# Kernel optimization log

Measured on AMD Instinct MI355X. Metric: run time of the kernel, lower is better.

The kernel has to match this reference:

```python
import jax, jax.numpy as jnp
import numpy as np

N = 100000
E = 3200000
H = 64

def _lin(k, fan_in, fan_out):
    k1, k2 = jax.random.split(k)
    lim = 1.0 / np.sqrt(fan_in)
    W = jax.random.uniform(k1, (fan_in, fan_out), minval=-lim, maxval=lim, dtype=jnp.float32)
    b = jax.random.uniform(k2, (fan_out,), minval=-lim, maxval=lim, dtype=jnp.float32)
    return W, b

def setup_inputs() -> dict:
    key = jax.random.key(0)
    ks = jax.random.split(key, 12)
    x = jax.random.normal(ks[0], (N, 6), dtype=jnp.float32)
    adj = jax.random.randint(ks[1], (2, E), 0, N, dtype=jnp.int64)
    W1, b1 = _lin(ks[2], 6, H)
    W2, b2 = _lin(ks[3], H, H)
    Wf1, bf1 = _lin(ks[4], H, H)
    Wf2, bf2 = _lin(ks[5], H, H)
    Ws1, bs1 = _lin(ks[6], H, 32)
    Ws2, bs2 = _lin(ks[7], 32, 1)
    Wt1, bt1 = _lin(ks[8], H, 32)
    Wt2, bt2 = _lin(ks[9], 32, 4)
    return dict(x=x, adj=adj, W1=W1, b1=b1, W2=W2, b2=b2, Wf1=Wf1, bf1=bf1,
                Wf2=Wf2, bf2=bf2, Ws1=Ws1, bs1=bs1, Ws2=Ws2, bs2=bs2,
                Wt1=Wt1, bt1=bt1, Wt2=Wt2, bt2=bt2)

def reference(x, adj, W1, b1, W2, b2, Wf1, bf1, Wf2, bf2,
              Ws1, bs1, Ws2, bs2, Wt1, bt1, Wt2, bt2):
    # cell encoder: Linear(6,H) -> ReLU -> Linear(H,H)
    h = jax.nn.relu(x @ W1 + b1) @ W2 + b2  # [N, H]
    # scatter-mean neighbor aggregation: neighbor_sum[i] = mean(h[adj[1][adj[0]==i]])
    src = adj[0]
    dst = adj[1]
    gathered = h[dst]  # [E, H]
    seg_sum = jax.ops.segment_sum(gathered, src, num_segments=N)  # [N, H]
    counts = jax.ops.segment_sum(jnp.ones((E,), dtype=h.dtype), src, num_segments=N)  # [N]
    neighbor_mean = seg_sum / jnp.maximum(counts, 1.0)[:, None]  # zero where no neighbors
    h = h + neighbor_mean
    h = jax.nn.relu(h @ Wf1 + bf1)
    h = jax.nn.relu(h @ Wf2 + bf2)
    error_scores = (jax.nn.relu(h @ Ws1 + bs1) @ Ws2 + bs2)[:, 0]  # [N]
    error_types = jax.nn.relu(h @ Wt1 + bt1) @ Wt2 + bt2  # [N, 4]
    return (error_scores, error_types)
```

## Files before the change

kernel.cpp:

```cpp
#include <hip/hip_runtime.h>
#include <hip/hip_fp16.h>

#define NN 100000
#define NE 3200000
#define H  64

#define BSHIFT 7
#define BNODES 128
#define NB ((NN + BNODES - 1) / BNODES)

#define PTHREADS 1024
#define PCHUNK   8192
#define PEPT     (PCHUNK / PTHREADS)
#define NPBLK    ((NE + PCHUNK - 1) / PCHUNK)

#define ECAP 5120

__global__ __launch_bounds__(256) void prepack_kernel(
    const float* __restrict__ W2,
    const float* __restrict__ Wf1, const float* __restrict__ Wf2,
    const float* __restrict__ Ws1, const float* __restrict__ bs1,
    const float* __restrict__ Ws2, const float* __restrict__ bs2,
    const float* __restrict__ Wt1, const float* __restrict__ bt1,
    const float* __restrict__ Wt2, const float* __restrict__ bt2,
    int* __restrict__ bfill,
    float* __restrict__ wf1t, float* __restrict__ wf2t,
    float* __restrict__ wht,  float* __restrict__ w2t,
    float* __restrict__ bhead, float* __restrict__ wfin, float* __restrict__ bfin)
{
    const int tid = threadIdx.x;
    if (blockIdx.x < 64) {
        const int e   = blockIdx.x * 256 + tid;
        const int a   = e >> 12;
        const int idx = e & 4095;
        const int k4  = idx >> 8;
        const int ff  = (idx >> 2) & 63;
        const int j   = idx & 3;
        if (a == 0)      wf1t[idx] = Wf1[k4 * 256 + j * 64 + ff];
        else if (a == 1) wf2t[idx] = Wf2[k4 * 256 + j * 64 + ff];
        else if (a == 2) wht[idx]  = (ff < 32) ? Ws1[k4 * 128 + j * 32 + ff]
                                               : Wt1[k4 * 128 + j * 32 + (ff - 32)];
        else             w2t[idx]  = W2[k4 * 256 + j * 64 + ff];
    } else {
        for (int i = tid; i < NB; i += 256) bfill[i] = 0;
        if (tid < 64) bhead[tid] = (tid < 32) ? bs1[tid] : bt1[tid - 32];
        if (tid < 160) {
            const int c = tid >> 5, jj = tid & 31;
            wfin[tid] = (c == 0) ? Ws2[jj] : Wt2[jj * 4 + (c - 1)];
        }
        if (tid < 5) bfin[tid] = (tid == 0) ? bs2[0] : bt2[tid - 1];
    }
}

__global__ __launch_bounds__(256) void encoder_kernel(
    const float* __restrict__ x,
    const float* __restrict__ W1, const float* __restrict__ b1,
    const float* __restrict__ w2t, const float* __restrict__ b2,
    __half* __restrict__ h16)
{
    __shared__ float sh[16][H];
    const int tid = threadIdx.x;
    const int w   = tid >> 6;
    const int f   = tid & 63;
    const int nw  = blockIdx.x * 16 + w * 4;

    const float xv = (f < 24) ? x[nw * 6 + f] : 0.0f;

    const float bb1 = b1[f];
    float w1r[6];
    #pragma unroll
    for (int k = 0; k < 6; ++k) w1r[k] = W1[k * H + f];

    #pragma unroll
    for (int j = 0; j < 4; ++j) {
        float acc = bb1;
        #pragma unroll
        for (int k = 0; k < 6; ++k)
            acc = fmaf(__shfl(xv, j * 6 + k), w1r[k], acc);
        sh[w * 4 + j][f] = fmaxf(acc, 0.0f);
    }
    const float bb2 = b2[f];
    float o0 = bb2, o1 = bb2, o2 = bb2, o3 = bb2;
    #pragma unroll
    for (int k4 = 0; k4 < 16; ++k4) {
        const float4 wv = *reinterpret_cast<const float4*>(&w2t[(k4 * 64 + f) * 4]);
        const float4 a0 = *reinterpret_cast<const float4*>(&sh[w * 4 + 0][k4 * 4]);
        const float4 a1 = *reinterpret_cast<const float4*>(&sh[w * 4 + 1][k4 * 4]);
        const float4 a2 = *reinterpret_cast<const float4*>(&sh[w * 4 + 2][k4 * 4]);
        const float4 a3 = *reinterpret_cast<const float4*>(&sh[w * 4 + 3][k4 * 4]);
        o0 = fmaf(a0.x, wv.x, o0); o0 = fmaf(a0.y, wv.y, o0); o0 = fmaf(a0.z, wv.z, o0); o0 = fmaf(a0.w, wv.w, o0);
        o1 = fmaf(a1.x, wv.x, o1); o1 = fmaf(a1.y, wv.y, o1); o1 = fmaf(a1.z, wv.z, o1); o1 = fmaf(a1.w, wv.w, o1);
        o2 = fmaf(a2.x, wv.x, o2); o2 = fmaf(a2.y, wv.y, o2); o2 = fmaf(a2.z, wv.z, o2); o2 = fmaf(a2.w, wv.w, o2);
        o3 = fmaf(a3.x, wv.x, o3); o3 = fmaf(a3.y, wv.y, o3); o3 = fmaf(a3.z, wv.z, o3); o3 = fmaf(a3.w, wv.w, o3);
    }
    h16[((size_t)(nw + 0) << 6) + f] = __float2half(o0);
    h16[((size_t)(nw + 1) << 6) + f] = __float2half(o1);
    h16[((size_t)(nw + 2) << 6) + f] = __float2half(o2);
    h16[((size_t)(nw + 3) << 6) + f] = __float2half(o3);
}

__global__ __launch_bounds__(PTHREADS) void partition_kernel(
    const int* __restrict__ src, const int* __restrict__ dst,
    int* __restrict__ bfill, unsigned* __restrict__ staging)
{
    __shared__ unsigned stage[PCHUNK];
    __shared__ int gpos[PCHUNK];
    __shared__ int lh[NB];
    __shared__ int lcur[NB];
    __shared__ int gbase[NB];
    __shared__ int wtot[16];
    const int t = threadIdx.x;
    const int lane = t & 63;
    const int wid  = t >> 6;
    const int cbase = blockIdx.x * PCHUNK;
    const int cnt = min(PCHUNK, NE - cbase);

    for (int i = t; i < NB; i += PTHREADS) lh[i] = 0;
    __syncthreads();

    unsigned ent[PEPT];
    int bkt[PEPT];
    const int tbase = t * PEPT;
    if (tbase + PEPT <= cnt) {
        const int4 s0 = *reinterpret_cast<const int4*>(&src[cbase + tbase]);
        const int4 s1 = *reinterpret_cast<const int4*>(&src[cbase + tbase + 4]);
        const int4 d0 = *reinterpret_cast<const int4*>(&dst[cbase + tbase]);
        const int4 d1 = *reinterpret_cast<const int4*>(&dst[cbase + tbase + 4]);
        const int sa_[8] = {s0.x, s0.y, s0.z, s0.w, s1.x, s1.y, s1.z, s1.w};
        const int da_[8] = {d0.x, d0.y, d0.z, d0.w, d1.x, d1.y, d1.z, d1.w};
        #pragma unroll
        for (int j = 0; j < PEPT; ++j) {
            bkt[j] = sa_[j] >> BSHIFT;
            ent[j] = (unsigned)da_[j] | ((unsigned)(sa_[j] & (BNODES - 1)) << 17);
            atomicAdd(&lh[bkt[j]], 1);
        }
    } else {
        #pragma unroll
        for (int j = 0; j < PEPT; ++j) {
            const int idx = tbase + j;
            if (idx < cnt) {
                const int s_ = src[cbase + idx];
                const int d_ = dst[cbase + idx];
                bkt[j] = s_ >> BSHIFT;
                ent[j] = (unsigned)d_ | ((unsigned)(s_ & (BNODES - 1)) << 17);
                atomicAdd(&lh[bkt[j]], 1);
            } else bkt[j] = -1;
        }
    }
    __syncthreads();

    const int hv = (t < NB) ? lh[t] : 0;
    int incl = hv;
    #pragma unroll
    for (int off = 1; off < 64; off <<= 1) {
        const int n = __shfl_up(incl, off);
        if (lane >= off) incl += n;
    }
    if (lane == 63) wtot[wid] = incl;
    __syncthreads();
    if (wid == 0 && lane < 16) {
        const int v = wtot[lane];
        int s2 = v;
        #pragma unroll
        for (int off = 1; off < 16; off <<= 1) {
            const int n = __shfl_up(s2, off);
            if (lane >= off) s2 += n;
        }
        wtot[lane] = s2 - v;
    }
    __syncthreads();
    if (t < NB) {
        const int excl = incl - hv + wtot[wid];
        lh[t]   = excl;
        lcur[t] = excl;
        gbase[t] = t * ECAP + ((hv > 0) ? atomicAdd(&bfill[t], hv) : 0);
    }
    __syncthreads();

    #pragma unroll
    for (int j = 0; j < PEPT; ++j) {
        if (bkt[j] >= 0) {
            const int lp = atomicAdd(&lcur[bkt[j]], 1);
            stage[lp] = ent[j];
            gpos[lp]  = gbase[bkt[j]] + (lp - lh[bkt[j]]);
        }
    }
    __syncthreads();

    for (int i = t; i < cnt; i += PTHREADS)
        staging[gpos[i]] = stage[i];
}

__global__ __launch_bounds__(1024) void bucket_sort_kernel(
    const unsigned* __restrict__ staging, const int* __restrict__ bfill,
    int* __restrict__ sdst, int* __restrict__ offs, int* __restrict__ counts)
{
    __shared__ int ldst[ECAP];
    __shared__ int cntS[BNODES];
    __shared__ int scanS[BNODES];
    __shared__ int lstart[BNODES];
    __shared__ int lcur[BNODES];
    const int t = threadIdx.x;
    const int b = blockIdx.x;
    const int base0 = b * ECAP;
    const int ecnt  = bfill[b];

    if (t < BNODES) cntS[t] = 0;
    __syncthreads();

    const uint4 e0 = *reinterpret_cast<const uint4*>(&staging[base0 + t * 4]);
    const uint4 e1 = *reinterpret_cast<const uint4*>(&staging[base0 + 4096 + t * 4]);
    const unsigned ev[8] = {e0.x, e0.y, e0.z, e0.w, e1.x, e1.y, e1.z, e1.w};
    int iv[8];
    #pragma unroll
    for (int u = 0; u < 8; ++u)
        iv[u] = (u < 4) ? (t * 4 + u) : (4096 + t * 4 + (u - 4));

    #pragma unroll
    for (int u = 0; u < 8; ++u)
        if (iv[u] < ecnt) atomicAdd(&cntS[ev[u] >> 17], 1);
    __syncthreads();

    if (t < BNODES) scanS[t] = (cntS[t] + 3) & ~3;
    __syncthreads();
    for (int off = 1; off < BNODES; off <<= 1) {
        int xv = 0;
        if (t >= off && t < BNODES) xv = scanS[t - off];
        __syncthreads();
        if (t >= off && t < BNODES) scanS[t] += xv;
        __syncthreads();
    }
    if (t < BNODES) {
        const int st = scanS[t] - ((cntS[t] + 3) & ~3);
        lstart[t] = st;
        lcur[t]   = st;
    }
    __syncthreads();

    #pragma unroll
    for (int u = 0; u < 8; ++u)
        if (iv[u] < ecnt) {
            const int lp = atomicAdd(&lcur[(int)(ev[u] >> 17)], 1);
            ldst[lp] = (int)(ev[u] & 0x1FFFFu);
        }
    __syncthreads();

    const int tot4 = scanS[BNODES - 1];
    for (int i = t * 4; i < tot4; i += 4096)
        *reinterpret_cast<int4*>(&sdst[base0 + i]) =
            *reinterpret_cast<const int4*>(&ldst[i]);

    const int nbase = b * BNODES;
    if (t < BNODES && nbase + t < NN) {
        offs[nbase + t]   = base0 + lstart[t];
        counts[nbase + t] = cntS[t];
    }
}

#define ACC4(cv, u)                                                            \
    {                                                                          \
        const float m = (rem > (u)) ? 1.0f : 0.0f;                             \
        const __half2* ph = reinterpret_cast<const __half2*>(&(cv));           \
        const float2 p0 = __half22float2(ph[0]);                               \
        const float2 p1 = __half22float2(ph[1]);                               \
        const float2 p2 = __half22float2(ph[2]);                               \
        const float2 p3 = __half22float2(ph[3]);                               \
        acc0 = fmaf(m, p0.x, acc0); acc1 = fmaf(m, p0.y, acc1);                \
        acc2 = fmaf(m, p1.x, acc2); acc3 = fmaf(m, p1.y, acc3);                \
        acc4 = fmaf(m, p2.x, acc4); acc5 = fmaf(m, p2.y, acc5);                \
        acc6 = fmaf(m, p3.x, acc6); acc7 = fmaf(m, p3.y, acc7);                \
    }

#define FLUSHN(jj)                                                             \
    {                                                                          \
        float4* w0 = reinterpret_cast<float4*>(&sp[wv][r][g << 3]);            \
        w0[0] = make_float4(acc0, acc1, acc2, acc3);                           \
        w0[1] = make_float4(acc4, acc5, acc6, acc7);                           \
        const float ssum = sp[wv][0][f] + sp[wv][1][f] + sp[wv][2][f]          \
                         + sp[wv][3][f] + sp[wv][4][f] + sp[wv][5][f]          \
                         + sp[wv][6][f] + sp[wv][7][f];                        \
        const int dgj = DGf(jj);                                               \
        sa[lb + jj][f] = SVf(jj) + ssum * (1.0f / fmaxf((float)dgj, 1.0f));    \
        acc0 = acc1 = acc2 = acc3 = acc4 = acc5 = acc6 = acc7 = 0.0f;          \
    }

#define GSTEP(c0, c1, c2, c3, n0_, n1_, n2_, n3_)                              \
    {                                                                          \
        if (jn < 4) {                       \
            const int rem = DGf(jn) - bn - 4 * r;                              \
            const int i0 = (rem > 0) ? idxN.x : 0;                             \
            const int i1 = (rem > 1) ? idxN.y : 0;                             \
            const int i2 = (rem > 2) ? idxN.z : 0;                             \
            const int i3 = (rem > 3) ? idxN.w : 0;                             \
            n0_ = *reinterpret_cast<const int4*>(hbase + ((size_t)i0 << 6));   \
            n1_ = *reinterpret_cast<const int4*>(hbase + ((size_t)i1 << 6));   \
            n2_ = *reinterpret_cast<const int4*>(hbase + ((size_t)i2 << 6));   \
            n3_ = *reinterpret_cast<const int4*>(hbase + ((size_t)i3 << 6));   \
        }                                                                      \
        int jm = jn, bm = bn; adv(jm, bm);                                     \
        idxN = IDXL(jm, bm);                                                   \
        {                                \
            const int rem = DGf(jc) - bc - 4 * r;                              \
            ACC4(c0, 0); ACC4(c1, 1); ACC4(c2, 2); ACC4(c3, 3);                \
        }                                                                      \
        if (jn != jc) FLUSHN(jc);                                              \
        jc = jn; bc = bn; jn = jm; bn = bm;                                    \
    }

__global__ __launch_bounds__(128, 4) void gather_head_kernel(
    const __half* __restrict__ h16,
    const int* __restrict__ counts, const int* __restrict__ offs,
    const int* __restrict__ sdst,
    const float* __restrict__ wf1t, const float* __restrict__ bf1,
    const float* __restrict__ wf2t, const float* __restrict__ bf2,
    const float* __restrict__ wht,  const float* __restrict__ bhead,
    const float* __restrict__ wfin, const float* __restrict__ bfin,
    float* __restrict__ out_scores, float* __restrict__ out_types)
{
    __shared__ float sa[8][H];
    __shared__ float sb[8][H];
    __shared__ float sp[2][8][H];
    const int f  = threadIdx.x & 63;
    const int wv = threadIdx.x >> 6;
    const int lb = wv * 4;
    const int n0 = blockIdx.x * 8 + lb;
    const int g  = f & 7;
    const int r  = f >> 3;
    const __half* __restrict__ hbase = h16 + (g << 3);

    const int dg0 = counts[n0 + 0], dg1 = counts[n0 + 1],
              dg2 = counts[n0 + 2], dg3 = counts[n0 + 3];
    const int st0 = offs[n0 + 0], st1 = offs[n0 + 1],
              st2 = offs[n0 + 2], st3 = offs[n0 + 3];

    const float sv0 = __half2float(h16[((size_t)(n0 + 0) << 6) + f]);
    const float sv1 = __half2float(h16[((size_t)(n0 + 1) << 6) + f]);
    const float sv2 = __half2float(h16[((size_t)(n0 + 2) << 6) + f]);
    const float sv3 = __half2float(h16[((size_t)(n0 + 3) << 6) + f]);
    sa[lb + 0][f] = sv0; sa[lb + 1][f] = sv1;
    sa[lb + 2][f] = sv2; sa[lb + 3][f] = sv3;

    auto DGf = [&](int j) { return j == 0 ? dg0 : j == 1 ? dg1 : j == 2 ? dg2 : dg3; };
    auto STf = [&](int j) { return j == 0 ? st0 : j == 1 ? st1 : j == 2 ? st2 : st3; };
    auto SVf = [&](int j) { return j == 0 ? sv0 : j == 1 ? sv1 : j == 2 ? sv2 : sv3; };
    auto adv = [&](int& j, int& b) {
        if (j >= 4) return;
        b += 32;
        if (b >= DGf(j)) { b = 0; do { ++j; } while (j < 4 && DGf(j) == 0); }
    };
    auto IDXL = [&](int j, int b) -> int4 {
        if (j < 4) return *reinterpret_cast<const int4*>(&sdst[STf(j) + b + 4 * r]);
        return make_int4(0, 0, 0, 0);
    };

    float acc0 = 0.f, acc1 = 0.f, acc2 = 0.f, acc3 = 0.f,
          acc4 = 0.f, acc5 = 0.f, acc6 = 0.f, acc7 = 0.f;
    int4 A0 = make_int4(0,0,0,0), A1 = A0, A2 = A0, A3 = A0;
    int4 B0 = A0, B1 = A0, B2 = A0, B3 = A0;

    int jc = 0, bc = 0;
    while (jc < 4 && DGf(jc) == 0) ++jc;
    int jn = jc, bn = bc; adv(jn, bn);
    int4 idxC = IDXL(jc, bc);
    int4 idxN = IDXL(jn, bn);
    if (jc < 4) {
        const int rem = DGf(jc) - bc - 4 * r;
        const int i0 = (rem > 0) ? idxC.x : 0;
        const int i1 = (rem > 1) ? idxC.y : 0;
        const int i2 = (rem > 2) ? idxC.z : 0;
        const int i3 = (rem > 3) ? idxC.w : 0;
        A0 = *reinterpret_cast<const int4*>(hbase + ((size_t)i0 << 6));
        A1 = *reinterpret_cast<const int4*>(hbase + ((size_t)i1 << 6));
        A2 = *reinterpret_cast<const int4*>(hbase + ((size_t)i2 << 6));
        A3 = *reinterpret_cast<const int4*>(hbase + ((size_t)i3 << 6));
    }

    while (jc < 4) {
        GSTEP(A0, A1, A2, A3, B0, B1, B2, B3);
        if (jc >= 4) break;
        GSTEP(B0, B1, B2, B3, A0, A1, A2, A3);
    }

    {
        const float bb = bf1[f];
        float o0 = bb, o1 = bb, o2 = bb, o3 = bb;
        #pragma unroll
        for (int k4 = 0; k4 < 16; ++k4) {
            const float4 w  = *reinterpret_cast<const float4*>(&wf1t[(k4 * 64 + f) * 4]);
            const float4 a0 = *reinterpret_cast<const float4*>(&sa[lb + 0][k4 * 4]);
            const float4 a1 = *reinterpret_cast<const float4*>(&sa[lb + 1][k4 * 4]);
            const float4 a2 = *reinterpret_cast<const float4*>(&sa[lb + 2][k4 * 4]);
            const float4 a3 = *reinterpret_cast<const float4*>(&sa[lb + 3][k4 * 4]);
            o0 = fmaf(a0.x, w.x, o0); o0 = fmaf(a0.y, w.y, o0); o0 = fmaf(a0.z, w.z, o0); o0 = fmaf(a0.w, w.w, o0);
            o1 = fmaf(a1.x, w.x, o1); o1 = fmaf(a1.y, w.y, o1); o1 = fmaf(a1.z, w.z, o1); o1 = fmaf(a1.w, w.w, o1);
            o2 = fmaf(a2.x, w.x, o2); o2 = fmaf(a2.y, w.y, o2); o2 = fmaf(a2.z, w.z, o2); o2 = fmaf(a2.w, w.w, o2);
            o3 = fmaf(a3.x, w.x, o3); o3 = fmaf(a3.y, w.y, o3); o3 = fmaf(a3.z, w.z, o3); o3 = fmaf(a3.w, w.w, o3);
        }
        sb[lb + 0][f] = fmaxf(o0, 0.0f);
        sb[lb + 1][f] = fmaxf(o1, 0.0f);
        sb[lb + 2][f] = fmaxf(o2, 0.0f);
        sb[lb + 3][f] = fmaxf(o3, 0.0f);
    }

    {
        const float bb = bf2[f];
        float o0 = bb, o1 = bb, o2 = bb, o3 = bb;
        #pragma unroll
        for (int k4 = 0; k4 < 16; ++k4) {
            const float4 w  = *reinterpret_cast<const float4*>(&wf2t[(k4 * 64 + f) * 4]);
            const float4 a0 = *reinterpret_cast<const float4*>(&sb[lb + 0][k4 * 4]);
            const float4 a1 = *reinterpret_cast<const float4*>(&sb[lb + 1][k4 * 4]);
            const float4 a2 = *reinterpret_cast<const float4*>(&sb[lb + 2][k4 * 4]);
            const float4 a3 = *reinterpret_cast<const float4*>(&sb[lb + 3][k4 * 4]);
            o0 = fmaf(a0.x, w.x, o0); o0 = fmaf(a0.y, w.y, o0); o0 = fmaf(a0.z, w.z, o0); o0 = fmaf(a0.w, w.w, o0);
            o1 = fmaf(a1.x, w.x, o1); o1 = fmaf(a1.y, w.y, o1); o1 = fmaf(a1.z, w.z, o1); o1 = fmaf(a1.w, w.w, o1);
            o2 = fmaf(a2.x, w.x, o2); o2 = fmaf(a2.y, w.y, o2); o2 = fmaf(a2.z, w.z, o2); o2 = fmaf(a2.w, w.w, o2);
            o3 = fmaf(a3.x, w.x, o3); o3 = fmaf(a3.y, w.y, o3); o3 = fmaf(a3.z, w.z, o3); o3 = fmaf(a3.w, w.w, o3);
        }
        sa[lb + 0][f] = fmaxf(o0, 0.0f);
        sa[lb + 1][f] = fmaxf(o1, 0.0f);
        sa[lb + 2][f] = fmaxf(o2, 0.0f);
        sa[lb + 3][f] = fmaxf(o3, 0.0f);
    }

    {
        const float bb = bhead[f];
        float o0 = bb, o1 = bb, o2 = bb, o3 = bb;
        #pragma unroll
        for (int k4 = 0; k4 < 16; ++k4) {
            const float4 w  = *reinterpret_cast<const float4*>(&wht[(k4 * 64 + f) * 4]);
            const float4 a0 = *reinterpret_cast<const float4*>(&sa[lb + 0][k4 * 4]);
            const float4 a1 = *reinterpret_cast<const float4*>(&sa[lb + 1][k4 * 4]);
            const float4 a2 = *reinterpret_cast<const float4*>(&sa[lb + 2][k4 * 4]);
            const float4 a3 = *reinterpret_cast<const float4*>(&sa[lb + 3][k4 * 4]);
            o0 = fmaf(a0.x, w.x, o0); o0 = fmaf(a0.y, w.y, o0); o0 = fmaf(a0.z, w.z, o0); o0 = fmaf(a0.w, w.w, o0);
            o1 = fmaf(a1.x, w.x, o1); o1 = fmaf(a1.y, w.y, o1); o1 = fmaf(a1.z, w.z, o1); o1 = fmaf(a1.w, w.w, o1);
            o2 = fmaf(a2.x, w.x, o2); o2 = fmaf(a2.y, w.y, o2); o2 = fmaf(a2.z, w.z, o2); o2 = fmaf(a2.w, w.w, o2);
            o3 = fmaf(a3.x, w.x, o3); o3 = fmaf(a3.y, w.y, o3); o3 = fmaf(a3.z, w.z, o3); o3 = fmaf(a3.w, w.w, o3);
        }
        sb[lb + 0][f] = fmaxf(o0, 0.0f);
        sb[lb + 1][f] = fmaxf(o1, 0.0f);
        sb[lb + 2][f] = fmaxf(o2, 0.0f);
        sb[lb + 3][f] = fmaxf(o3, 0.0f);
    }

    {
        const int j = f >> 4;
        const int c = f & 15;
        if (c < 5) {
            float a2 = bfin[c];
            const int off = (c == 0) ? 0 : 32;
            const int rot = ((c << 2) + (j << 3)) & 31;
            #pragma unroll 8
            for (int jj = 0; jj < 32; ++jj) {
                const int q = (jj + rot) & 31;
                a2 = fmaf(sb[lb + j][off + q], wfin[c * 32 + q], a2);
            }
            const int node = n0 + j;
            if (c == 0) out_scores[node] = a2;
            else        out_types[node * 4 + (c - 1)] = a2;
        }
    }
}

#undef GSTEP
#undef FLUSHN
#undef ACC4

extern "C" void kernel_launch(void* const* d_in, const int* in_sizes, int n_in,
                              void* d_out, int out_size, void* d_ws, size_t ws_size,
                              hipStream_t stream)
{
    const float* x   = (const float*)d_in[0];
    const int*   adj = (const int*)  d_in[1];
    const float* W1  = (const float*)d_in[2];
    const float* b1  = (const float*)d_in[3];
    const float* W2  = (const float*)d_in[4];
    const float* b2  = (const float*)d_in[5];
    const float* Wf1 = (const float*)d_in[6];
    const float* bf1 = (const float*)d_in[7];
    const float* Wf2 = (const float*)d_in[8];
    const float* bf2 = (const float*)d_in[9];
    const float* Ws1 = (const float*)d_in[10];
    const float* bs1 = (const float*)d_in[11];
    const float* Ws2 = (const float*)d_in[12];
    const float* bs2 = (const float*)d_in[13];
    const float* Wt1 = (const float*)d_in[14];
    const float* bt1 = (const float*)d_in[15];
    const float* Wt2 = (const float*)d_in[16];
    const float* bt2 = (const float*)d_in[17];

    float* out_scores = (float*)d_out;
    float* out_types  = out_scores + NN;

    unsigned* staging = (unsigned*)d_ws;
    int*      sdst    = (int*)(staging + (size_t)NB * ECAP);
    __half*   h16     = (__half*)(sdst + (size_t)NB * ECAP);
    int*      counts  = (int*)(h16 + (size_t)NN * H);
    int*      offs    = counts + NN;
    int*      bfill   = offs + NN;
    float*    wf1t    = (float*)(bfill + 784);
    float*    wf2t    = wf1t + 4096;
    float*    wht     = wf2t + 4096;
    float*    w2t     = wht + 4096;
    float*    bhead   = w2t + 4096;
    float*    wfin    = bhead + 64;
    float*    bfin    = wfin + 160;

    const int* src = adj;
    const int* dst = adj + NE;

    prepack_kernel<<<65, 256, 0, stream>>>(W2, Wf1, Wf2, Ws1, bs1, Ws2, bs2,
                                           Wt1, bt1, Wt2, bt2,
                                           bfill, wf1t, wf2t, wht, w2t,
                                           bhead, wfin, bfin);
    encoder_kernel<<<NN / 16, 256, 0, stream>>>(x, W1, b1, w2t, b2, h16);
    partition_kernel<<<NPBLK, PTHREADS, 0, stream>>>(src, dst, bfill, staging);
    bucket_sort_kernel<<<NB, 1024, 0, stream>>>(staging, bfill, sdst, offs, counts);
    gather_head_kernel<<<NN / 8, 128, 0, stream>>>(h16, counts, offs, sdst,
                                                   wf1t, bf1, wf2t, bf2,
                                                   wht, bhead, wfin, bfin,
                                                   out_scores, out_types);
}
```

Before: 261.0 us.

## Deepen gather prefetch to three stages and use single-wave blocks

The neighbor gather loop now rotates three register buffers instead of two, so two batches of fp16 neighbor rows are in flight while a third is being accumulated. The gather/head kernel also drops to 64-thread single-wavefront blocks handling 4 nodes each, which removes the per-wave shared-memory indexing. Separately, the bucket sort skips the second staging load when a bucket holds at most 4096 edges. The deeper pipeline raises register use, which may lower occupancy, and it doubles the number of blocks launched.

```diff
diff --git a/kernel.cpp b/kernel.cpp
--- a/kernel.cpp
+++ b/kernel.cpp
@@ -209,7 +209,9 @@
     __syncthreads();
 
     const uint4 e0 = *reinterpret_cast<const uint4*>(&staging[base0 + t * 4]);
-    const uint4 e1 = *reinterpret_cast<const uint4*>(&staging[base0 + 4096 + t * 4]);
+    uint4 e1 = make_uint4(0u, 0u, 0u, 0u);
+    if (ecnt > 4096)
+        e1 = *reinterpret_cast<const uint4*>(&staging[base0 + 4096 + t * 4]);
     const unsigned ev[8] = {e0.x, e0.y, e0.z, e0.w, e1.x, e1.y, e1.z, e1.w};
     int iv[8];
     #pragma unroll
@@ -273,41 +275,45 @@
 
 #define FLUSHN(jj)                                                             \
     {                                                                          \
-        float4* w0 = reinterpret_cast<float4*>(&sp[wv][r][g << 3]);            \
+        float4* w0 = reinterpret_cast<float4*>(&sp[r][g << 3]);                \
         w0[0] = make_float4(acc0, acc1, acc2, acc3);                           \
         w0[1] = make_float4(acc4, acc5, acc6, acc7);                           \
-        const float ssum = sp[wv][0][f] + sp[wv][1][f] + sp[wv][2][f]          \
-                         + sp[wv][3][f] + sp[wv][4][f] + sp[wv][5][f]          \
-                         + sp[wv][6][f] + sp[wv][7][f];                        \
+        const float ssum = sp[0][f] + sp[1][f] + sp[2][f] + sp[3][f]           \
+                         + sp[4][f] + sp[5][f] + sp[6][f] + sp[7][f];          \
         const int dgj = DGf(jj);                                               \
-        sa[lb + jj][f] = SVf(jj) + ssum * (1.0f / fmaxf((float)dgj, 1.0f));    \
+        sa[jj][f] = SVf(jj) + ssum * (1.0f / fmaxf((float)dgj, 1.0f));         \
         acc0 = acc1 = acc2 = acc3 = acc4 = acc5 = acc6 = acc7 = 0.0f;          \
     }
 
-#define GSTEP(c0, c1, c2, c3, n0_, n1_, n2_, n3_)                              \
+#define FILLB(n0_, n1_, n2_, n3_, jF, bF, idxF)                                \
+    if ((jF) < 4) {                                                            \
+        const int rem = DGf(jF) - (bF) - 4 * r;                                \
+        const int i0 = (rem > 0) ? (idxF).x : 0;                               \
+        const int i1 = (rem > 1) ? (idxF).y : 0;                               \
+        const int i2 = (rem > 2) ? (idxF).z : 0;                               \
+        const int i3 = (rem > 3) ? (idxF).w : 0;                               \
+        n0_ = *reinterpret_cast<const int4*>(hbase + ((size_t)i0 << 6));       \
+        n1_ = *reinterpret_cast<const int4*>(hbase + ((size_t)i1 << 6));       \
+        n2_ = *reinterpret_cast<const int4*>(hbase + ((size_t)i2 << 6));       \
+        n3_ = *reinterpret_cast<const int4*>(hbase + ((size_t)i3 << 6));       \
+    }
+
+#define STEP3(c0, c1, c2, c3, d0_, d1_, d2_, d3_)                              \
     {                                                                          \
-        if (jn < 4) {                       \
-            const int rem = DGf(jn) - bn - 4 * r;                              \
-            const int i0 = (rem > 0) ? idxN.x : 0;                             \
-            const int i1 = (rem > 1) ? idxN.y : 0;                             \
-            const int i2 = (rem > 2) ? idxN.z : 0;                             \
-            const int i3 = (rem > 3) ? idxN.w : 0;                             \
-            n0_ = *reinterpret_cast<const int4*>(hbase + ((size_t)i0 << 6));   \
-            n1_ = *reinterpret_cast<const int4*>(hbase + ((size_t)i1 << 6));   \
-            n2_ = *reinterpret_cast<const int4*>(hbase + ((size_t)i2 << 6));   \
-            n3_ = *reinterpret_cast<const int4*>(hbase + ((size_t)i3 << 6));   \
-        }                                                                      \
-        int jm = jn, bm = bn; adv(jm, bm);                                     \
-        idxN = IDXL(jm, bm);                                                   \
-        {                                \
+        FILLB(d0_, d1_, d2_, d3_, j2, b2, idxQ);                               \
+        int j4 = j3, b4 = b3; adv(j4, b4);                                     \
+        const int4 idxN = IDXL(j4, b4);                                        \
+        {                                                                      \
             const int rem = DGf(jc) - bc - 4 * r;                              \
             ACC4(c0, 0); ACC4(c1, 1); ACC4(c2, 2); ACC4(c3, 3);                \
         }                                                                      \
-        if (jn != jc) FLUSHN(jc);                                              \
-        jc = jn; bc = bn; jn = jm; bn = bm;                                    \
-    }
-
-__global__ __launch_bounds__(128, 4) void gather_head_kernel(
+        if (j1 != jc) FLUSHN(jc);                                              \
+        jc = j1; bc = b1; j1 = j2; b1 = b2;                                    \
+        j2 = j3; b2 = b3; j3 = j4; b3 = b4;                                    \
+        idxQ = idxQ2; idxQ2 = idxN;                                            \
+    }
+
+__global__ __launch_bounds__(64, 4) void gather_head_kernel(
     const __half* __restrict__ h16,
     const int* __restrict__ counts, const int* __restrict__ offs,
     const int* __restrict__ sdst,
@@ -317,13 +323,11 @@
     const float* __restrict__ wfin, const float* __restrict__ bfin,
     float* __restrict__ out_scores, float* __restrict__ out_types)
 {
-    __shared__ float sa[8][H];
-    __shared__ float sb[8][H];
-    __shared__ float sp[2][8][H];
-    const int f  = threadIdx.x & 63;
-    const int wv = threadIdx.x >> 6;
-    const int lb = wv * 4;
-    const int n0 = blockIdx.x * 8 + lb;
+    __shared__ float sa[4][H];
+    __shared__ float sb[4][H];
+    __shared__ float sp[8][H];
+    const int f  = threadIdx.x;
+    const int n0 = blockIdx.x * 4;
     const int g  = f & 7;
     const int r  = f >> 3;
     const __half* __restrict__ hbase = h16 + (g << 3);
@@ -337,8 +341,7 @@
     const float sv1 = __half2float(h16[((size_t)(n0 + 1) << 6) + f]);
     const float sv2 = __half2float(h16[((size_t)(n0 + 2) << 6) + f]);
     const float sv3 = __half2float(h16[((size_t)(n0 + 3) << 6) + f]);
-    sa[lb + 0][f] = sv0; sa[lb + 1][f] = sv1;
-    sa[lb + 2][f] = sv2; sa[lb + 3][f] = sv3;
+    sa[0][f] = sv0; sa[1][f] = sv1; sa[2][f] = sv2; sa[3][f] = sv3;
 
     auto DGf = [&](int j) { return j == 0 ? dg0 : j == 1 ? dg1 : j == 2 ? dg2 : dg3; };
     auto STf = [&](int j) { return j == 0 ? st0 : j == 1 ? st1 : j == 2 ? st2 : st3; };
@@ -357,28 +360,26 @@
           acc4 = 0.f, acc5 = 0.f, acc6 = 0.f, acc7 = 0.f;
     int4 A0 = make_int4(0,0,0,0), A1 = A0, A2 = A0, A3 = A0;
     int4 B0 = A0, B1 = A0, B2 = A0, B3 = A0;
+    int4 C0 = A0, C1 = A0, C2 = A0, C3 = A0;
 
     int jc = 0, bc = 0;
     while (jc < 4 && DGf(jc) == 0) ++jc;
-    int jn = jc, bn = bc; adv(jn, bn);
-    int4 idxC = IDXL(jc, bc);
-    int4 idxN = IDXL(jn, bn);
-    if (jc < 4) {
-        const int rem = DGf(jc) - bc - 4 * r;
-        const int i0 = (rem > 0) ? idxC.x : 0;
-        const int i1 = (rem > 1) ? idxC.y : 0;
-        const int i2 = (rem > 2) ? idxC.z : 0;
-        const int i3 = (rem > 3) ? idxC.w : 0;
-        A0 = *reinterpret_cast<const int4*>(hbase + ((size_t)i0 << 6));
-        A1 = *reinterpret_cast<const int4*>(hbase + ((size_t)i1 << 6));
-        A2 = *reinterpret_cast<const int4*>(hbase + ((size_t)i2 << 6));
-        A3 = *reinterpret_cast<const int4*>(hbase + ((size_t)i3 << 6));
-    }
+    int j1 = jc, b1 = bc; adv(j1, b1);
+    int j2 = j1, b2 = b1; adv(j2, b2);
+    int j3 = j2, b3 = b2; adv(j3, b3);
+    const int4 idx0 = IDXL(jc, bc);
+    const int4 idx1 = IDXL(j1, b1);
+    int4 idxQ  = IDXL(j2, b2);
+    int4 idxQ2 = IDXL(j3, b3);
+    FILLB(A0, A1, A2, A3, jc, bc, idx0);
+    FILLB(B0, B1, B2, B3, j1, b1, idx1);
 
     while (jc < 4) {
-        GSTEP(A0, A1, A2, A3, B0, B1, B2, B3);
+        STEP3(A0, A1, A2, A3, C0, C1, C2, C3);
         if (jc >= 4) break;
-        GSTEP(B0, B1, B2, B3, A0, A1, A2, A3);
+        STEP3(B0, B1, B2, B3, A0, A1, A2, A3);
+        if (jc >= 4) break;
+        STEP3(C0, C1, C2, C3, B0, B1, B2, B3);
     }
 
     {
@@ -387,19 +388,19 @@
         #pragma unroll
         for (int k4 = 0; k4 < 16; ++k4) {
             const float4 w  = *reinterpret_cast<const float4*>(&wf1t[(k4 * 64 + f) * 4]);
-            const float4 a0 = *reinterpret_cast<const float4*>(&sa[lb + 0][k4 * 4]);
-            const float4 a1 = *reinterpret_cast<const float4*>(&sa[lb + 1][k4 * 4]);
-            const float4 a2 = *reinterpret_cast<const float4*>(&sa[lb + 2][k4 * 4]);
-            const float4 a3 = *reinterpret_cast<const float4*>(&sa[lb + 3][k4 * 4]);
+            const float4 a0 = *reinterpret_cast<const float4*>(&sa[0][k4 * 4]);
+            const float4 a1 = *reinterpret_cast<const float4*>(&sa[1][k4 * 4]);
+            const float4 a2 = *reinterpret_cast<const float4*>(&sa[2][k4 * 4]);
+            const float4 a3 = *reinterpret_cast<const float4*>(&sa[3][k4 * 4]);
             o0 = fmaf(a0.x, w.x, o0); o0 = fmaf(a0.y, w.y, o0); o0 = fmaf(a0.z, w.z, o0); o0 = fmaf(a0.w, w.w, o0);
             o1 = fmaf(a1.x, w.x, o1); o1 = fmaf(a1.y, w.y, o1); o1 = fmaf(a1.z, w.z, o1); o1 = fmaf(a1.w, w.w, o1);
             o2 = fmaf(a2.x, w.x, o2); o2 = fmaf(a2.y, w.y, o2); o2 = fmaf(a2.z, w.z, o2); o2 = fmaf(a2.w, w.w, o2);
             o3 = fmaf(a3.x, w.x, o3); o3 = fmaf(a3.y, w.y, o3); o3 = fmaf(a3.z, w.z, o3); o3 = fmaf(a3.w, w.w, o3);
         }
-        sb[lb + 0][f] = fmaxf(o0, 0.0f);
-        sb[lb + 1][f] = fmaxf(o1, 0.0f);
-        sb[lb + 2][f] = fmaxf(o2, 0.0f);
-        sb[lb + 3][f] = fmaxf(o3, 0.0f);
+        sb[0][f] = fmaxf(o0, 0.0f);
+        sb[1][f] = fmaxf(o1, 0.0f);
+        sb[2][f] = fmaxf(o2, 0.0f);
+        sb[3][f] = fmaxf(o3, 0.0f);
     }
 
     {
@@ -408,19 +409,19 @@
         #pragma unroll
         for (int k4 = 0; k4 < 16; ++k4) {
             const float4 w  = *reinterpret_cast<const float4*>(&wf2t[(k4 * 64 + f) * 4]);
-            const float4 a0 = *reinterpret_cast<const float4*>(&sb[lb + 0][k4 * 4]);
-            const float4 a1 = *reinterpret_cast<const float4*>(&sb[lb + 1][k4 * 4]);
-            const float4 a2 = *reinterpret_cast<const float4*>(&sb[lb + 2][k4 * 4]);
-            const float4 a3 = *reinterpret_cast<const float4*>(&sb[lb + 3][k4 * 4]);
+            const float4 a0 = *reinterpret_cast<const float4*>(&sb[0][k4 * 4]);
+            const float4 a1 = *reinterpret_cast<const float4*>(&sb[1][k4 * 4]);
+            const float4 a2 = *reinterpret_cast<const float4*>(&sb[2][k4 * 4]);
+            const float4 a3 = *reinterpret_cast<const float4*>(&sb[3][k4 * 4]);
             o0 = fmaf(a0.x, w.x, o0); o0 = fmaf(a0.y, w.y, o0); o0 = fmaf(a0.z, w.z, o0); o0 = fmaf(a0.w, w.w, o0);
             o1 = fmaf(a1.x, w.x, o1); o1 = fmaf(a1.y, w.y, o1); o1 = fmaf(a1.z, w.z, o1); o1 = fmaf(a1.w, w.w, o1);
             o2 = fmaf(a2.x, w.x, o2); o2 = fmaf(a2.y, w.y, o2); o2 = fmaf(a2.z, w.z, o2); o2 = fmaf(a2.w, w.w, o2);
             o3 = fmaf(a3.x, w.x, o3); o3 = fmaf(a3.y, w.y, o3); o3 = fmaf(a3.z, w.z, o3); o3 = fmaf(a3.w, w.w, o3);
         }
-        sa[lb + 0][f] = fmaxf(o0, 0.0f);
-        sa[lb + 1][f] = fmaxf(o1, 0.0f);
-        sa[lb + 2][f] = fmaxf(o2, 0.0f);
-        sa[lb + 3][f] = fmaxf(o3, 0.0f);
+        sa[0][f] = fmaxf(o0, 0.0f);
+        sa[1][f] = fmaxf(o1, 0.0f);
+        sa[2][f] = fmaxf(o2, 0.0f);
+        sa[3][f] = fmaxf(o3, 0.0f);
     }
 
     {
@@ -429,19 +430,19 @@
         #pragma unroll
         for (int k4 = 0; k4 < 16; ++k4) {
             const float4 w  = *reinterpret_cast<const float4*>(&wht[(k4 * 64 + f) * 4]);
-            const float4 a0 = *reinterpret_cast<const float4*>(&sa[lb + 0][k4 * 4]);
-            const float4 a1 = *reinterpret_cast<const float4*>(&sa[lb + 1][k4 * 4]);
-            const float4 a2 = *reinterpret_cast<const float4*>(&sa[lb + 2][k4 * 4]);
-            const float4 a3 = *reinterpret_cast<const float4*>(&sa[lb + 3][k4 * 4]);
+            const float4 a0 = *reinterpret_cast<const float4*>(&sa[0][k4 * 4]);
+            const float4 a1 = *reinterpret_cast<const float4*>(&sa[1][k4 * 4]);
+            const float4 a2 = *reinterpret_cast<const float4*>(&sa[2][k4 * 4]);
+            const float4 a3 = *reinterpret_cast<const float4*>(&sa[3][k4 * 4]);
             o0 = fmaf(a0.x, w.x, o0); o0 = fmaf(a0.y, w.y, o0); o0 = fmaf(a0.z, w.z, o0); o0 = fmaf(a0.w, w.w, o0);
             o1 = fmaf(a1.x, w.x, o1); o1 = fmaf(a1.y, w.y, o1); o1 = fmaf(a1.z, w.z, o1); o1 = fmaf(a1.w, w.w, o1);
             o2 = fmaf(a2.x, w.x, o2); o2 = fmaf(a2.y, w.y, o2); o2 = fmaf(a2.z, w.z, o2); o2 = fmaf(a2.w, w.w, o2);
             o3 = fmaf(a3.x, w.x, o3); o3 = fmaf(a3.y, w.y, o3); o3 = fmaf(a3.z, w.z, o3); o3 = fmaf(a3.w, w.w, o3);
         }
-        sb[lb + 0][f] = fmaxf(o0, 0.0f);
-        sb[lb + 1][f] = fmaxf(o1, 0.0f);
-        sb[lb + 2][f] = fmaxf(o2, 0.0f);
-        sb[lb + 3][f] = fmaxf(o3, 0.0f);
+        sb[0][f] = fmaxf(o0, 0.0f);
+        sb[1][f] = fmaxf(o1, 0.0f);
+        sb[2][f] = fmaxf(o2, 0.0f);
+        sb[3][f] = fmaxf(o3, 0.0f);
     }
 
     {
@@ -454,7 +455,7 @@
             #pragma unroll 8
             for (int jj = 0; jj < 32; ++jj) {
                 const int q = (jj + rot) & 31;
-                a2 = fmaf(sb[lb + j][off + q], wfin[c * 32 + q], a2);
+                a2 = fmaf(sb[j][off + q], wfin[c * 32 + q], a2);
             }
             const int node = n0 + j;
             if (c == 0) out_scores[node] = a2;
@@ -463,7 +464,8 @@
     }
 }
 
-#undef GSTEP
+#undef STEP3
+#undef FILLB
 #undef FLUSHN
 #undef ACC4
 
@@ -517,8 +519,8 @@
     encoder_kernel<<<NN / 16, 256, 0, stream>>>(x, W1, b1, w2t, b2, h16);
     partition_kernel<<<NPBLK, PTHREADS, 0, stream>>>(src, dst, bfill, staging);
     bucket_sort_kernel<<<NB, 1024, 0, stream>>>(staging, bfill, sdst, offs, counts);
-    gather_head_kernel<<<NN / 8, 128, 0, stream>>>(h16, counts, offs, sdst,
-                                                   wf1t, bf1, wf2t, bf2,
-                                                   wht, bhead, wfin, bfin,
-                                                   out_scores, out_types);
+    gather_head_kernel<<<NN / 4, 64, 0, stream>>>(h16, counts, offs, sdst,
+                                                  wf1t, bf1, wf2t, bf2,
+                                                  wht, bhead, wfin, bfin,
+                                                  out_scores, out_types);
 }
```

Result: faster. 244.4 us (-6.4%).
